# Kernel tuning notes

Measured on AMD Instinct MI355X. Metric: run time of the kernel, lower is better.

Reference implementation:

```python
import jax, jax.numpy as jnp
import numpy as np

D_MODEL = 1024
N_HEAD = 16
HEAD_DIM = D_MODEL // N_HEAD
ROPE_BASE = 10000.0


def _weight_quant(w):
    # BitNet b1.58 ternary weight quant with per-tensor absmean scale (STE).
    scale = jnp.clip(jnp.mean(jnp.abs(w)), 1e-5, None)
    wq = jnp.clip(jnp.round(w / scale), -1.0, 1.0) * scale
    return w + jax.lax.stop_gradient(wq - w)


def _act_quant(x):
    # Per-token int8 absmax activation quant (STE).
    scale = 127.0 / jnp.clip(jnp.max(jnp.abs(x), axis=-1, keepdims=True), 1e-5, None)
    xq = jnp.clip(jnp.round(x * scale), -128.0, 127.0) / scale
    return x + jax.lax.stop_gradient(xq - x)


def _bitlinear(x, w):
    # y = act_quant(x) @ weight_quant(w).T   (torch Linear convention, no bias)
    return _act_quant(x) @ _weight_quant(w).T


def _rope(x, pos):
    # x: [B, H, T, D]; half-split rotation.
    d = x.shape[-1]
    inv_freq = 1.0 / (ROPE_BASE ** (jnp.arange(0, d, 2, dtype=jnp.float32) / d))
    ang = pos[:, None].astype(jnp.float32) * inv_freq[None, :]  # [T, D/2]
    cos, sin = jnp.cos(ang), jnp.sin(ang)
    x1, x2 = x[..., : d // 2], x[..., d // 2 :]
    return jnp.concatenate([x1 * cos - x2 * sin, x1 * sin + x2 * cos], axis=-1)


def setup_inputs() -> dict:
    key = jax.random.key(0)
    k0, k1, k2, k3, k4 = jax.random.split(key, 5)
    B, T = 2, 2048
    s = 1.0 / np.sqrt(D_MODEL)
    return {
        "x": jax.random.normal(k0, (B, T, D_MODEL), dtype=jnp.float32),
        "Wq": jax.random.normal(k1, (D_MODEL, D_MODEL), dtype=jnp.float32) * s,
        "Wk": jax.random.normal(k2, (D_MODEL, D_MODEL), dtype=jnp.float32) * s,
        "Wv": jax.random.normal(k3, (D_MODEL, D_MODEL), dtype=jnp.float32) * s,
        "Wo": jax.random.normal(k4, (D_MODEL, D_MODEL), dtype=jnp.float32) * s,
    }


def reference(x, Wq, Wk, Wv, Wo):
    B, T, C = x.shape
    pos = jnp.arange(T)
    def heads(y):
        return y.reshape(B, T, N_HEAD, HEAD_DIM).transpose(0, 2, 1, 3)  # [B,H,T,D]
    q = _rope(heads(_bitlinear(x, Wq)), pos)
    k = _rope(heads(_bitlinear(x, Wk)), pos)
    v = heads(_bitlinear(x, Wv))
    scores = jnp.einsum("bhqd,bhkd->bhqk", q, k) / jnp.sqrt(jnp.float32(HEAD_DIM))
    causal = jnp.tril(jnp.ones((T, T), dtype=bool))
    scores = jnp.where(causal[None, None], scores, jnp.finfo(scores.dtype).min)
    att = jax.nn.softmax(scores, axis=-1)
    y = jnp.einsum("bhqk,bhkd->bhqd", att, v)  # [B,H,T,D]
    y = y.transpose(0, 2, 1, 3).reshape(B, T, C)
    return _bitlinear(y, Wo)
```

## Files before the change

### kernel.cpp

```cpp
#include <hip/hip_runtime.h>
#include <hip/hip_bf16.h>
#include <math.h>

typedef __bf16 bf16_t;
typedef signed char i8_t;
typedef __attribute__((ext_vector_type(8))) __bf16 bf16x8;
typedef __attribute__((ext_vector_type(4))) __bf16 bf16x4;
typedef __attribute__((ext_vector_type(4))) float f32x4;
typedef __attribute__((ext_vector_type(4))) int i32x4;

typedef __attribute__((address_space(3))) void lds_void_t;
typedef const __attribute__((address_space(1))) void glb_void_t;
#define GLOAD_LDS(g, l) __builtin_amdgcn_global_load_lds((glb_void_t*)(g), (lds_void_t*)(l), 16, 0, 0)

#define MFMA16(a,b,c) __builtin_amdgcn_mfma_f32_16x16x32_bf16(a,b,c,0,0,0)
#define MFMAI8(a,b,c) __builtin_amdgcn_mfma_i32_16x16x64_i8(a,b,c,0,0,0)

#if __has_builtin(__builtin_amdgcn_exp2f)
#define EXP2F(x) __builtin_amdgcn_exp2f(x)
#else
#define EXP2F(x) exp2f(x)
#endif

static constexpr int TSEQ = 2048;
static constexpr int CDIM = 1024;
#define NEG_BIG (-1.0e30f)
#define Q_PRESCALE 0.18033688011112042f
#define ROPE_C 0.41524101190971284f

__global__ __launch_bounds__(256) void wreduce(const float* __restrict__ W0, const float* __restrict__ W1,
                                               const float* __restrict__ W2, const float* __restrict__ W3,
                                               double* __restrict__ partial) {
  int w = blockIdx.x >> 6, b = blockIdx.x & 63;
  const float* W = (w==0)?W0:(w==1)?W1:(w==2)?W2:W3;
  const float* base = W + (size_t)b * 16384;
  double s = 0.0;
  for (int i = threadIdx.x * 4; i < 16384; i += 1024) {
    float4 v = *(const float4*)(base + i);
    s += (double)fabsf(v.x) + (double)fabsf(v.y) + (double)fabsf(v.z) + (double)fabsf(v.w);
  }
  #pragma unroll
  for (int off = 1; off < 64; off <<= 1) s += __shfl_xor(s, off);
  __shared__ double red[4];
  if ((threadIdx.x & 63) == 0) red[threadIdx.x >> 6] = s;
  __syncthreads();
  if (threadIdx.x == 0) partial[blockIdx.x] = red[0] + red[1] + red[2] + red[3];
}

__global__ __launch_bounds__(256) void prep(const float* __restrict__ W0, const float* __restrict__ W1,
                                            const float* __restrict__ W2, const float* __restrict__ W3,
                                            const double* __restrict__ partial, float* __restrict__ wscale,
                                            i8_t* __restrict__ wq_all,
                                            const float* __restrict__ xg, i8_t* __restrict__ xqg,
                                            float* __restrict__ rowfac, float2* __restrict__ ropetab) {
  int bid = blockIdx.x;
  if (bid < 4096) {
    int w = bid >> 10;
    double ssum = 0.0;
    for (int i = 0; i < 64; ++i) ssum += partial[w * 64 + i];
    float s = fmaxf((float)(ssum * (1.0 / 1048576.0)), 1e-5f);
    if ((bid & 1023) == 0 && threadIdx.x == 0) wscale[w] = s;
    const float* W = (w==0)?W0:(w==1)?W1:(w==2)?W2:W3;
    int off = ((bid & 1023) * 256 + threadIdx.x) * 4;
    float4 v = *(const float4*)(W + off);
    char4 q;
    q.x = (i8_t)(int)fminf(fmaxf(rintf(v.x / s), -1.f), 1.f);
    q.y = (i8_t)(int)fminf(fmaxf(rintf(v.y / s), -1.f), 1.f);
    q.z = (i8_t)(int)fminf(fmaxf(rintf(v.z / s), -1.f), 1.f);
    q.w = (i8_t)(int)fminf(fmaxf(rintf(v.w / s), -1.f), 1.f);
    *(char4*)(wq_all + (size_t)w * 1048576 + off) = q;
  } else if (bid < 8192) {
    int r = bid - 4096;
    float4 v = *(const float4*)(xg + (size_t)r * 1024 + threadIdx.x * 4);
    float mx = fmaxf(fmaxf(fabsf(v.x), fabsf(v.y)), fmaxf(fabsf(v.z), fabsf(v.w)));
    #pragma unroll
    for (int off = 1; off < 64; off <<= 1) mx = fmaxf(mx, __shfl_xor(mx, off));
    __shared__ float red[4];
    if ((threadIdx.x & 63) == 0) red[threadIdx.x >> 6] = mx;
    __syncthreads();
    mx = fmaxf(fmaxf(red[0], red[1]), fmaxf(red[2], red[3]));
    mx = fmaxf(mx, 1e-5f);
    float scale = 127.0f / mx;
    if (threadIdx.x == 0) rowfac[r] = mx * (1.0f / 127.0f);
    char4 q;
    q.x = (i8_t)(int)fminf(fmaxf(rintf(v.x * scale), -128.f), 127.f);
    q.y = (i8_t)(int)fminf(fmaxf(rintf(v.y * scale), -128.f), 127.f);
    q.z = (i8_t)(int)fminf(fmaxf(rintf(v.z * scale), -128.f), 127.f);
    q.w = (i8_t)(int)fminf(fmaxf(rintf(v.w * scale), -128.f), 127.f);
    *(char4*)(xqg + (size_t)r * 1024 + threadIdx.x * 4) = q;
  } else {
    int t = (bid - 8192) * 8 + (threadIdx.x >> 5);
    int ii = threadIdx.x & 31;
    float ang = (float)t * exp2f(-(float)ii * ROPE_C);
    float sn, cs;
    sincosf(ang, &sn, &cs);
    ropetab[t * 32 + ii] = make_float2(cs, sn);
  }
}

__global__ __launch_bounds__(256) void actquant(const float* __restrict__ xg, i8_t* __restrict__ xqg,
                                                float* __restrict__ rowfac) {
  int r = blockIdx.x;
  float4 v = *(const float4*)(xg + (size_t)r * 1024 + threadIdx.x * 4);
  float mx = fmaxf(fmaxf(fabsf(v.x), fabsf(v.y)), fmaxf(fabsf(v.z), fabsf(v.w)));
  #pragma unroll
  for (int off = 1; off < 64; off <<= 1) mx = fmaxf(mx, __shfl_xor(mx, off));
  __shared__ float red[4];
  if ((threadIdx.x & 63) == 0) red[threadIdx.x >> 6] = mx;
  __syncthreads();
  mx = fmaxf(fmaxf(red[0], red[1]), fmaxf(red[2], red[3]));
  mx = fmaxf(mx, 1e-5f);
  float scale = 127.0f / mx;
  if (threadIdx.x == 0) rowfac[r] = mx * (1.0f / 127.0f);
  char4 q;
  q.x = (i8_t)(int)fminf(fmaxf(rintf(v.x * scale), -128.f), 127.f);
  q.y = (i8_t)(int)fminf(fmaxf(rintf(v.y * scale), -128.f), 127.f);
  q.z = (i8_t)(int)fminf(fmaxf(rintf(v.z * scale), -128.f), 127.f);
  q.w = (i8_t)(int)fminf(fmaxf(rintf(v.w * scale), -128.f), 127.f);
  *(char4*)(xqg + (size_t)r * 1024 + threadIdx.x * 4) = q;
}

__global__ __launch_bounds__(256) void gemm_qkv(const i8_t* __restrict__ xq, const i8_t* __restrict__ wq_all,
                                                const float* __restrict__ wscale, const float* __restrict__ rowfac,
                                                const float2* __restrict__ ropetab,
                                                bf16_t* __restrict__ qb, bf16_t* __restrict__ kb,
                                                bf16_t* __restrict__ vtb) {
  const int z = blockIdx.z;
  const i8_t* Bw = wq_all + (size_t)z * 1048576;
  const int m0 = blockIdx.x * 128, n0 = blockIdx.y * 128;
  const int tid = threadIdx.x;
  const int wave = tid >> 6, lane = tid & 63, quad = lane >> 4, l16 = lane & 15;
  const int wm = wave >> 1, wn = wave & 1;
  __shared__ __align__(16) i8_t As[128 * 64];
  __shared__ __align__(16) i8_t Bs[128 * 64];
  i32x4 zero = {0, 0, 0, 0};
  i32x4 acc[4][4];
  #pragma unroll
  for (int i = 0; i < 4; ++i)
    #pragma unroll
    for (int j = 0; j < 4; ++j) acc[i][j] = zero;

  const int row_s = tid >> 2;
  const int cg16 = (((tid & 3) - (row_s >> 1)) & 3) * 16;
  const int sw16 = ((quad + (l16 >> 1)) & 3) * 16;

  for (int kt = 0; kt < 16; ++kt) {
    __syncthreads();
    #pragma unroll
    for (int v2 = 0; v2 < 2; ++v2) {
      int v = tid + v2 * 256;
      int row = row_s + v2 * 64;
      GLOAD_LDS(&xq[(size_t)(m0 + row) * 1024 + kt * 64 + cg16], &As[v * 16]);
      GLOAD_LDS(&Bw[(size_t)(n0 + row) * 1024 + kt * 64 + cg16], &Bs[v * 16]);
    }
    __syncthreads();
    i32x4 af[4], bfr[4];
    #pragma unroll
    for (int i = 0; i < 4; ++i) af[i] = *(const i32x4*)&As[(wm * 64 + i * 16 + l16) * 64 + sw16];
    #pragma unroll
    for (int j = 0; j < 4; ++j) bfr[j] = *(const i32x4*)&Bs[(wn * 64 + j * 16 + l16) * 64 + sw16];
    if (z == 2) {
      #pragma unroll
      for (int i = 0; i < 4; ++i)
        #pragma unroll
        for (int j = 0; j < 4; ++j) acc[i][j] = MFMAI8(bfr[i], af[j], acc[i][j]);
    } else {
      #pragma unroll
      for (int i = 0; i < 4; ++i)
        #pragma unroll
        for (int j = 0; j < 4; ++j) acc[i][j] = MFMAI8(af[i], bfr[j], acc[i][j]);
    }
  }
  float ws = wscale[z] * (z == 0 ? Q_PRESCALE : 1.0f);
  if (z <= 1) {
    bf16_t* dst = (z == 0) ? qb : kb;
    const int h = (n0 >> 6) + wn;
    #pragma unroll
    for (int i = 0; i < 4; ++i) {
      #pragma unroll
      for (int r = 0; r < 4; ++r) {
        int m = m0 + wm * 64 + i * 16 + quad * 4 + r;
        float rf = rowfac[m] * ws;
        int b = m >> 11, t = m & 2047;
        bf16_t* drow = dst + (((size_t)b * 16 + h) * 2048 + t) * 64;
        #pragma unroll
        for (int j = 0; j < 2; ++j) {
          int dd1 = j * 16 + l16;
          float2 cs2 = ropetab[t * 32 + dd1];
          float v1 = (float)acc[i][j][r] * rf;
          float v2 = (float)acc[i][j + 2][r] * rf;
          drow[dd1]      = (bf16_t)(v1 * cs2.x - v2 * cs2.y);
          drow[dd1 + 32] = (bf16_t)(v1 * cs2.y + v2 * cs2.x);
        }
      }
    }
  } else {
    const int b = m0 >> 11;
    const int tbase = (m0 & 2047) + wm * 64;
    float rfj[4];
    #pragma unroll
    for (int j = 0; j < 4; ++j) rfj[j] = rowfac[m0 + wm * 64 + j * 16 + l16] * ws;
    #pragma unroll
    for (int i = 0; i < 4; ++i) {
      #pragma unroll
      for (int r = 0; r < 4; ++r) {
        int nrow = n0 + wn * 64 + i * 16 + quad * 4 + r;
        int h = nrow >> 6, dd = nrow & 63;
        bf16_t* vrow = vtb + (((size_t)b * 16 + h) * 64 + dd) * 2048 + tbase;
        #pragma unroll
        for (int j = 0; j < 4; ++j) vrow[j * 16 + l16] = (bf16_t)((float)acc[i][j][r] * rfj[j]);
      }
    }
  }
}

__global__ __launch_bounds__(256) void gemm_out(const i8_t* __restrict__ yq, const i8_t* __restrict__ wo,
                                                const float* __restrict__ wscale, const float* __restrict__ rowfac,
                                                float* __restrict__ out) {
  const int m0 = blockIdx.x * 128, n0 = blockIdx.y * 128;
  const int tid = threadIdx.x;
  const int wave = tid >> 6, lane = tid & 63, quad = lane >> 4, l16 = lane & 15;
  const int wm = wave >> 1, wn = wave & 1;
  __shared__ __align__(16) i8_t As[128 * 64];
  __shared__ __align__(16) i8_t Bs[128 * 64];
  i32x4 zero = {0, 0, 0, 0};
  i32x4 acc[4][4];
  #pragma unroll
  for (int i = 0; i < 4; ++i)
    #pragma unroll
    for (int j = 0; j < 4; ++j) acc[i][j] = zero;

  const int row_s = tid >> 2;
  const int cg16 = (((tid & 3) - (row_s >> 1)) & 3) * 16;
  const int sw16 = ((quad + (l16 >> 1)) & 3) * 16;

  for (int kt = 0; kt < 16; ++kt) {
    __syncthreads();
    #pragma unroll
    for (int v2 = 0; v2 < 2; ++v2) {
      int v = tid + v2 * 256;
      int row = row_s + v2 * 64;
      GLOAD_LDS(&yq[(size_t)(m0 + row) * 1024 + kt * 64 + cg16], &As[v * 16]);
      GLOAD_LDS(&wo[(size_t)(n0 + row) * 1024 + kt * 64 + cg16], &Bs[v * 16]);
    }
    __syncthreads();
    i32x4 af[4], bfr[4];
    #pragma unroll
    for (int i = 0; i < 4; ++i) af[i] = *(const i32x4*)&As[(wm * 64 + i * 16 + l16) * 64 + sw16];
    #pragma unroll
    for (int j = 0; j < 4; ++j) bfr[j] = *(const i32x4*)&Bs[(wn * 64 + j * 16 + l16) * 64 + sw16];
    #pragma unroll
    for (int i = 0; i < 4; ++i)
      #pragma unroll
      for (int j = 0; j < 4; ++j) acc[i][j] = MFMAI8(af[i], bfr[j], acc[i][j]);
  }
  float ws = wscale[3];
  #pragma unroll
  for (int i = 0; i < 4; ++i) {
    #pragma unroll
    for (int r = 0; r < 4; ++r) {
      int m = m0 + wm * 64 + i * 16 + quad * 4 + r;
      float rf = rowfac[m] * ws;
      #pragma unroll
      for (int j = 0; j < 4; ++j) {
        int n = n0 + wn * 64 + j * 16 + l16;
        out[(size_t)m * 1024 + n] = (float)acc[i][j][r] * rf;
      }
    }
  }
}

__global__ __launch_bounds__(512) void flash_attn(const bf16_t* __restrict__ qg, const bf16_t* __restrict__ kg,
                                                  const bf16_t* __restrict__ vtg, float* __restrict__ yf) {
  const int lid = (int)blockIdx.y * 8 + (int)blockIdx.x;
  const int p  = (lid >> 3) & 7;
  const int bh = (lid & 7) * 4 + (lid >> 6);
  const int tid = threadIdx.x;
  const int wave = tid >> 6, lane = tid & 63;
  const int quad = lane >> 4, l16 = lane & 15;

  __shared__ __align__(16) bf16_t Kb[2][64 * 64];
  __shared__ __align__(16) bf16_t Vb[2][64 * 64];
  __shared__ __align__(16) bf16_t Pl[8][16 * 72];

  const int b = bh >> 4, h = bh & 15;
  bf16_t* Pw = &Pl[wave][0];

  const int r0 = tid >> 3, cblk = tid & 7;
  const int ldsOff0 = r0 * 64 + ((cblk ^ (r0 & 7)) * 8);
  const size_t bhbase = (size_t)bh * 131072;
  const bf16_t* kbase0 = kg + bhbase + r0 * 64 + cblk * 8;
  const bf16_t* vbase0 = vtg + bhbase + r0 * 2048 + cblk * 8;

  int kf_off[4][2];
  #pragma unroll
  for (int n = 0; n < 4; ++n)
    #pragma unroll
    for (int c = 0; c < 2; ++c)
      kf_off[n][c] = (n * 16 + l16) * 64 + (((c * 4 + quad) ^ (l16 & 7)) * 8);

  bf16x8 ones;
  #pragma unroll
  for (int j = 0; j < 8; ++j) ones[j] = (bf16_t)1.0f;
  f32x4 zero = {0.f, 0.f, 0.f, 0.f};

  bf16x8 kpre = *(const bf16x8*)(kbase0);
  bf16x8 vpre = *(const bf16x8*)(vbase0);

  int cum = 0;
  #pragma unroll 1
  for (int tsel = 0; tsel < 2; ++tsel) {
    const int qt = tsel ? (15 - p) : p;
    const int kcmax = 2 * qt + 1;
    const int qbw = qt * 128 + wave * 16;

    const bf16_t* qrowp = qg + ((size_t)bh * TSEQ + qbw + l16) * 64;
    bf16x8 aq0 = *(const bf16x8*)(qrowp + quad * 8);
    bf16x8 aq1 = *(const bf16x8*)(qrowp + 32 + quad * 8);

    f32x4 o[4], o5;
    #pragma unroll
    for (int i = 0; i < 4; ++i) o[i] = zero;
    o5 = zero;

    #pragma unroll 1
    for (int kc = 0; kc <= kcmax; ++kc, ++cum) {
      const int buf = cum & 1;
      bf16_t* Kt = &Kb[buf][0];
      bf16_t* Vt = &Vb[buf][0];
      *(bf16x8*)&Kt[ldsOff0] = kpre;
      *(bf16x8*)&Vt[ldsOff0] = vpre;
      __syncthreads();
      int nkc = (kc < kcmax) ? (kc + 1) : ((tsel == 0) ? 0 : -1);
      if (nkc >= 0) {
        kpre = *(const bf16x8*)(kbase0 + nkc * 4096);
        vpre = *(const bf16x8*)(vbase0 + nkc * 64);
      }

      if (kc * 64 > qbw + 15) continue;

      f32x4 s[4];
      __builtin_amdgcn_s_setprio(1);
      #pragma unroll
      for (int n = 0; n < 4; ++n) {
        bf16x8 bk0 = *(const bf16x8*)&Kt[kf_off[n][0]];
        bf16x8 bk1 = *(const bf16x8*)&Kt[kf_off[n][1]];
        s[n] = MFMA16(aq1, bk1, MFMA16(aq0, bk0, zero));
      }
      __builtin_amdgcn_s_setprio(0);
      if (kc * 64 + 63 > qbw) {
        #pragma unroll
        for (int n = 0; n < 4; ++n)
          #pragma unroll
          for (int r = 0; r < 4; ++r) {
            int kpos = kc * 64 + n * 16 + l16;
            int qpos = qbw + quad * 4 + r;
            if (kpos > qpos) s[n][r] = NEG_BIG;
          }
      }
      #pragma unroll
      for (int n = 0; n < 4; ++n)
        #pragma unroll
        for (int r = 0; r < 4; ++r)
          Pw[(quad * 4 + r) * 72 + n * 16 + l16] = (bf16_t)EXP2F(s[n][r]);

      bf16x8 ap0 = *(const bf16x8*)&Pw[l16 * 72 + quad * 8];
      bf16x8 ap1 = *(const bf16x8*)&Pw[l16 * 72 + 32 + quad * 8];
      __builtin_amdgcn_s_setprio(1);
      #pragma unroll
      for (int nh = 0; nh < 4; ++nh) {
        bf16x8 bv0 = *(const bf16x8*)&Vt[kf_off[nh][0]];
        bf16x8 bv1 = *(const bf16x8*)&Vt[kf_off[nh][1]];
        o[nh] = MFMA16(ap1, bv1, MFMA16(ap0, bv0, o[nh]));
      }
      o5 = MFMA16(ap1, ones, MFMA16(ap0, ones, o5));
      __builtin_amdgcn_s_setprio(0);
    }

    #pragma unroll
    for (int r = 0; r < 4; ++r) {
      float invl = 1.0f / o5[r];
      int t = qbw + quad * 4 + r;
      float* yrow = yf + ((size_t)b * TSEQ + t) * CDIM + h * 64;
      #pragma unroll
      for (int nh = 0; nh < 4; ++nh) yrow[nh * 16 + l16] = o[nh][r] * invl;
    }
  }
}

extern "C" void kernel_launch(void* const* d_in, const int* in_sizes, int n_in,
                              void* d_out, int out_size, void* d_ws, size_t ws_size,
                              hipStream_t stream) {
  const float* x  = (const float*)d_in[0];
  const float* Wq = (const float*)d_in[1];
  const float* Wk = (const float*)d_in[2];
  const float* Wv = (const float*)d_in[3];
  const float* Wo = (const float*)d_in[4];
  float* out = (float*)d_out;

  char* ws = (char*)d_ws;
  double* wpartial = (double*)(ws);
  float* wscale   = (float*)(ws + 4096);
  float* rowfacx  = (float*)(ws + 8192);
  float* rowfacy  = (float*)(ws + 8192 + 16384);
  i8_t* wq_all    = (i8_t*)(ws + 65536);
  i8_t* xq        = wq_all + 4194304;
  bf16_t* qb      = (bf16_t*)(xq + 4194304);
  bf16_t* kb      = qb + 4194304;
  bf16_t* vtb     = kb + 4194304;
  float*  yf      = (float*)(vtb + 4194304);
  float2* ropetab = (float2*)(yf + 4194304);
  i8_t* yq        = xq;

  wreduce<<<256, 256, 0, stream>>>(Wq, Wk, Wv, Wo, wpartial);
  prep<<<8448, 256, 0, stream>>>(Wq, Wk, Wv, Wo, wpartial, wscale, wq_all, x, xq, rowfacx, ropetab);
  gemm_qkv<<<dim3(32, 8, 3), 256, 0, stream>>>(xq, wq_all, wscale, rowfacx, ropetab, qb, kb, vtb);
  flash_attn<<<dim3(8, 32), 512, 0, stream>>>(qb, kb, vtb, yf);
  actquant<<<4096, 256, 0, stream>>>(yf, yq, rowfacy);
  gemm_out<<<dim3(32, 8), 256, 0, stream>>>(yq, wq_all + 3 * 1048576, wscale, rowfacy, out);
}
```

Measured before the change: 179.4 us.

## Triple-buffer LDS tiles in int8 GEMMs with async prefetch two stages ahead

Both int8 GEMM kernels (QKV projection and output projection) move from a single LDS buffer, synchronised twice per k-step, to a three-stage ring. Global-to-LDS loads are issued two k-tiles ahead, with explicit vmcnt waits and one barrier per iteration. This is meant to hide global load latency behind the MFMA work. In exchange, LDS use per block grows from 16KB to 48KB, which may limit occupancy, and correctness depends on the hand-counted waitcnt values.

```diff
diff --git a/kernel.cpp b/kernel.cpp
--- a/kernel.cpp
+++ b/kernel.cpp
@@ -21,6 +21,9 @@
 #else
 #define EXP2F(x) exp2f(x)
 #endif
+
+#define WAIT_VM4() do { asm volatile("s_waitcnt vmcnt(4) lgkmcnt(0)" ::: "memory"); __builtin_amdgcn_sched_barrier(0); } while (0)
+#define WAIT_VM0() do { asm volatile("s_waitcnt vmcnt(0) lgkmcnt(0)" ::: "memory"); __builtin_amdgcn_sched_barrier(0); } while (0)
 
 static constexpr int TSEQ = 2048;
 static constexpr int CDIM = 1024;
@@ -131,8 +134,8 @@
   const int tid = threadIdx.x;
   const int wave = tid >> 6, lane = tid & 63, quad = lane >> 4, l16 = lane & 15;
   const int wm = wave >> 1, wn = wave & 1;
-  __shared__ __align__(16) i8_t As[128 * 64];
-  __shared__ __align__(16) i8_t Bs[128 * 64];
+  __shared__ __align__(16) i8_t As[3][128 * 64];
+  __shared__ __align__(16) i8_t Bs[3][128 * 64];
   i32x4 zero = {0, 0, 0, 0};
   i32x4 acc[4][4];
   #pragma unroll
@@ -144,21 +147,31 @@
   const int cg16 = (((tid & 3) - (row_s >> 1)) & 3) * 16;
   const int sw16 = ((quad + (l16 >> 1)) & 3) * 16;
 
-  for (int kt = 0; kt < 16; ++kt) {
-    __syncthreads();
+  auto issue = [&](int kt) {
+    int buf = kt % 3;
     #pragma unroll
     for (int v2 = 0; v2 < 2; ++v2) {
       int v = tid + v2 * 256;
       int row = row_s + v2 * 64;
-      GLOAD_LDS(&xq[(size_t)(m0 + row) * 1024 + kt * 64 + cg16], &As[v * 16]);
-      GLOAD_LDS(&Bw[(size_t)(n0 + row) * 1024 + kt * 64 + cg16], &Bs[v * 16]);
-    }
-    __syncthreads();
+      GLOAD_LDS(&xq[(size_t)(m0 + row) * 1024 + kt * 64 + cg16], &As[buf][v * 16]);
+      GLOAD_LDS(&Bw[(size_t)(n0 + row) * 1024 + kt * 64 + cg16], &Bs[buf][v * 16]);
+    }
+  };
+
+  issue(0);
+  issue(1);
+  WAIT_VM4();
+  __builtin_amdgcn_s_barrier();
+
+  #pragma unroll 1
+  for (int kt = 0; kt < 16; ++kt) {
+    const int cur = kt % 3;
+    if (kt + 2 < 16) issue(kt + 2);
     i32x4 af[4], bfr[4];
     #pragma unroll
-    for (int i = 0; i < 4; ++i) af[i] = *(const i32x4*)&As[(wm * 64 + i * 16 + l16) * 64 + sw16];
-    #pragma unroll
-    for (int j = 0; j < 4; ++j) bfr[j] = *(const i32x4*)&Bs[(wn * 64 + j * 16 + l16) * 64 + sw16];
+    for (int i = 0; i < 4; ++i) af[i] = *(const i32x4*)&As[cur][(wm * 64 + i * 16 + l16) * 64 + sw16];
+    #pragma unroll
+    for (int j = 0; j < 4; ++j) bfr[j] = *(const i32x4*)&Bs[cur][(wn * 64 + j * 16 + l16) * 64 + sw16];
     if (z == 2) {
       #pragma unroll
       for (int i = 0; i < 4; ++i)
@@ -170,6 +183,9 @@
         #pragma unroll
         for (int j = 0; j < 4; ++j) acc[i][j] = MFMAI8(af[i], bfr[j], acc[i][j]);
     }
+    if (kt < 14) { WAIT_VM4(); }
+    else         { WAIT_VM0(); }
+    __builtin_amdgcn_s_barrier();
   }
   float ws = wscale[z] * (z == 0 ? Q_PRESCALE : 1.0f);
   if (z <= 1) {
@@ -221,8 +237,8 @@
   const int tid = threadIdx.x;
   const int wave = tid >> 6, lane = tid & 63, quad = lane >> 4, l16 = lane & 15;
   const int wm = wave >> 1, wn = wave & 1;
-  __shared__ __align__(16) i8_t As[128 * 64];
-  __shared__ __align__(16) i8_t Bs[128 * 64];
+  __shared__ __align__(16) i8_t As[3][128 * 64];
+  __shared__ __align__(16) i8_t Bs[3][128 * 64];
   i32x4 zero = {0, 0, 0, 0};
   i32x4 acc[4][4];
   #pragma unroll
@@ -234,25 +250,38 @@
   const int cg16 = (((tid & 3) - (row_s >> 1)) & 3) * 16;
   const int sw16 = ((quad + (l16 >> 1)) & 3) * 16;
 
-  for (int kt = 0; kt < 16; ++kt) {
-    __syncthreads();
+  auto issue = [&](int kt) {
+    int buf = kt % 3;
     #pragma unroll
     for (int v2 = 0; v2 < 2; ++v2) {
       int v = tid + v2 * 256;
       int row = row_s + v2 * 64;
-      GLOAD_LDS(&yq[(size_t)(m0 + row) * 1024 + kt * 64 + cg16], &As[v * 16]);
-      GLOAD_LDS(&wo[(size_t)(n0 + row) * 1024 + kt * 64 + cg16], &Bs[v * 16]);
-    }
-    __syncthreads();
+      GLOAD_LDS(&yq[(size_t)(m0 + row) * 1024 + kt * 64 + cg16], &As[buf][v * 16]);
+      GLOAD_LDS(&wo[(size_t)(n0 + row) * 1024 + kt * 64 + cg16], &Bs[buf][v * 16]);
+    }
+  };
+
+  issue(0);
+  issue(1);
+  WAIT_VM4();
+  __builtin_amdgcn_s_barrier();
+
+  #pragma unroll 1
+  for (int kt = 0; kt < 16; ++kt) {
+    const int cur = kt % 3;
+    if (kt + 2 < 16) issue(kt + 2);
     i32x4 af[4], bfr[4];
     #pragma unroll
-    for (int i = 0; i < 4; ++i) af[i] = *(const i32x4*)&As[(wm * 64 + i * 16 + l16) * 64 + sw16];
-    #pragma unroll
-    for (int j = 0; j < 4; ++j) bfr[j] = *(const i32x4*)&Bs[(wn * 64 + j * 16 + l16) * 64 + sw16];
+    for (int i = 0; i < 4; ++i) af[i] = *(const i32x4*)&As[cur][(wm * 64 + i * 16 + l16) * 64 + sw16];
+    #pragma unroll
+    for (int j = 0; j < 4; ++j) bfr[j] = *(const i32x4*)&Bs[cur][(wn * 64 + j * 16 + l16) * 64 + sw16];
     #pragma unroll
     for (int i = 0; i < 4; ++i)
       #pragma unroll
       for (int j = 0; j < 4; ++j) acc[i][j] = MFMAI8(af[i], bfr[j], acc[i][j]);
+    if (kt < 14) { WAIT_VM4(); }
+    else         { WAIT_VM0(); }
+    __builtin_amdgcn_s_barrier();
   }
   float ws = wscale[3];
   #pragma unroll
```

New measurement: 182.5 us. Within noise of the previous version (+1.7%).
